# Performance work log

Measured on AMD Instinct MI355X. Metric: run time of the kernel, lower is better.

The kernel has to match this reference:

```python
import jax, jax.numpy as jnp
import numpy as np

N_NODES = 40000
N_EDGES = 640000
D = 128
BN_EPS = 1e-5


def setup_inputs() -> dict:
    key = jax.random.key(0)
    ks = jax.random.split(key, 8)
    h = jax.random.normal(ks[0], (N_NODES, D), dtype=jnp.float32)
    snorm_n = jax.random.uniform(ks[1], (N_NODES, 1), dtype=jnp.float32)
    W_self = jax.random.normal(ks[2], (D, D), dtype=jnp.float32) * 0.05
    W_neigh = jax.random.normal(ks[3], (D, D), dtype=jnp.float32) * 0.05
    b = jax.random.normal(ks[4], (D,), dtype=jnp.float32) * 0.05
    gamma = jnp.ones((D,), dtype=jnp.float32)
    beta = jnp.zeros((D,), dtype=jnp.float32)
    src = jax.random.randint(ks[5], (N_EDGES,), 0, N_NODES, dtype=jnp.int32)
    dst = jax.random.randint(ks[6], (N_EDGES,), 0, N_NODES, dtype=jnp.int32)
    return {"h": h, "snorm_n": snorm_n, "W_self": W_self, "W_neigh": W_neigh,
            "b": b, "gamma": gamma, "beta": beta, "src": src, "dst": dst}


def reference(h, snorm_n, W_self, W_neigh, b, gamma, beta, src, dst):
    h_in = h
    # --- SAGEConv (mean aggregator): mean over in-neighbors (src -> dst) ---
    msg = h[src]                                   # [E, D] irregular gather
    agg = jax.ops.segment_sum(msg, dst, num_segments=N_NODES)  # [N, D]
    deg = jax.ops.segment_sum(jnp.ones((N_EDGES,), h.dtype), dst,
                              num_segments=N_NODES)            # [N]
    h_neigh = agg / jnp.maximum(deg, 1.0)[:, None]
    out = h @ W_self + h_neigh @ W_neigh + b       # fc_self + fc_neigh + bias
    out = jax.nn.relu(out)                         # activation
    # --- graph norm ---
    out = out * snorm_n
    # --- batch norm (training-style batch statistics over nodes) ---
    mean = jnp.mean(out, axis=0)
    var = jnp.var(out, axis=0)
    out = (out - mean) * jax.lax.rsqrt(var + BN_EPS) * gamma + beta
    # --- residual ---
    return h_in + out
```

## Files before the change

### kernel.cpp

```cpp
#include <hip/hip_runtime.h>
#include <hip/hip_bf16.h>

constexpr int N_NODES = 40000;
constexpr int N_EDGES = 640000;
constexpr int D = 128;
constexpr float BN_EPS = 1e-5f;
constexpr int CAP = 128;
constexpr int NTILES = 1250;
constexpr int NCOLOR = 8;
constexpr int NODES_PER_COLOR = N_NODES / NCOLOR;
constexpr int FILL_BLOCKS = 2560;
constexpr int COLOR_STRIDE = (FILL_BLOCKS / NCOLOR) * 256;
constexpr int NREP = 8;

typedef __attribute__((ext_vector_type(8))) short short8;
typedef __attribute__((ext_vector_type(4))) float f32x4;
typedef __attribute__((ext_vector_type(2))) float f32x2;

__device__ __forceinline__ unsigned bf16_rne(float f) {
    unsigned b = __float_as_uint(f);
    return (b + 0x7FFFu + ((b >> 16) & 1u)) >> 16;
}
__device__ __forceinline__ float bflo(unsigned w) { return __uint_as_float(w << 16); }
__device__ __forceinline__ float bfhi(unsigned w) { return __uint_as_float(w & 0xFFFF0000u); }

__global__ __launch_bounds__(256) void cvt_fill_kernel(
        const int* __restrict__ dst,
        const int* __restrict__ src,
        int* __restrict__ cursor,
        int* __restrict__ esrc,
        const float4* __restrict__ h4,
        uint4* __restrict__ hb4,
        uint2* __restrict__ hb8,
        const float* __restrict__ Wself,
        const float* __restrict__ Wneigh,
        uint4* __restrict__ wfrag) {
    int gid = blockIdx.x * blockDim.x + threadIdx.x;

    if (gid < N_EDGES) {
        float4 a = h4[2 * gid];
        float4 b = h4[2 * gid + 1];
        uint4 o;
        o.x = bf16_rne(a.x) | (bf16_rne(a.y) << 16);
        o.y = bf16_rne(a.z) | (bf16_rne(a.w) << 16);
        o.z = bf16_rne(b.x) | (bf16_rne(b.y) << 16);
        o.w = bf16_rne(b.z) | (bf16_rne(b.w) << 16);
        hb4[gid] = o;
        unsigned w0 = __builtin_amdgcn_cvt_pk_fp8_f32(a.x, a.y, 0, false);
        w0 = __builtin_amdgcn_cvt_pk_fp8_f32(a.z, a.w, w0, true);
        unsigned w1 = __builtin_amdgcn_cvt_pk_fp8_f32(b.x, b.y, 0, false);
        w1 = __builtin_amdgcn_cvt_pk_fp8_f32(b.z, b.w, w1, true);
        uint2 o8; o8.x = w0; o8.y = w1;
        hb8[gid] = o8;
    }
    if (gid < 4096) {
        int G = gid;
        int l = G & 63;
        int tile = G >> 6;
        int kg = l >> 4, n = l & 15;
        int ct = tile >> 3, kt = tile & 7;
        int k0 = kt * 32 + kg * 8;
        int col = ct * 16 + n;
        unsigned w[8];
        #pragma unroll
        for (int j = 0; j < 8; j++) {
            int k = k0 + j;
            float v = (k < D) ? Wself[(size_t)k * D + col]
                              : Wneigh[(size_t)(k - D) * D + col];
            w[j] = bf16_rne(v);
        }
        uint4 ow;
        ow.x = w[0] | (w[1] << 16);
        ow.y = w[2] | (w[3] << 16);
        ow.z = w[4] | (w[5] << 16);
        ow.w = w[6] | (w[7] << 16);
        wfrag[G] = ow;
    }

    int c = blockIdx.x & (NCOLOR - 1);
    int lo = c * NODES_PER_COLOR;
    int hi = lo + NODES_PER_COLOR;
    int base = (blockIdx.x >> 3) * 256 + threadIdx.x;
    for (int e = base; e < N_EDGES; e += COLOR_STRIDE) {
        int t = dst[e];
        if (t >= lo && t < hi) {
            int s = src[e];
            int p = atomicAdd(&cursor[t], 1);
            if (p < CAP) esrc[t * CAP + p] = s;
        }
    }
}

__global__ __launch_bounds__(256) void gather_kernel(
        const uint4* __restrict__ hb8q,
        const int* __restrict__ cursor,
        const int* __restrict__ esrc,
        uint4* __restrict__ hnb4) {
    int c = blockIdx.x & (NCOLOR - 1);
    int rank = blockIdx.x >> 3;
    int wid = threadIdx.x >> 6;
    int node = c * NODES_PER_COLOR + rank * 4 + wid;
    int lane = threadIdx.x & 63;
    int g  = lane & 7;
    int es = lane >> 3;
    int deg = cursor[node];
    int cnt = deg < CAP ? deg : CAP;
    const int* bucket = esrc + node * CAP;
    float acc[16];
    #pragma unroll
    for (int i = 0; i < 16; i++) acc[i] = 0.f;
    for (int j = es; j < cnt; j += 8) {
        int a = bucket[j];
        uint4 v = hb8q[(size_t)a * 8 + g];
        f32x2 f;
        f = __builtin_amdgcn_cvt_pk_f32_fp8(v.x, false); acc[0]  += f.x; acc[1]  += f.y;
        f = __builtin_amdgcn_cvt_pk_f32_fp8(v.x, true);  acc[2]  += f.x; acc[3]  += f.y;
        f = __builtin_amdgcn_cvt_pk_f32_fp8(v.y, false); acc[4]  += f.x; acc[5]  += f.y;
        f = __builtin_amdgcn_cvt_pk_f32_fp8(v.y, true);  acc[6]  += f.x; acc[7]  += f.y;
        f = __builtin_amdgcn_cvt_pk_f32_fp8(v.z, false); acc[8]  += f.x; acc[9]  += f.y;
        f = __builtin_amdgcn_cvt_pk_f32_fp8(v.z, true);  acc[10] += f.x; acc[11] += f.y;
        f = __builtin_amdgcn_cvt_pk_f32_fp8(v.w, false); acc[12] += f.x; acc[13] += f.y;
        f = __builtin_amdgcn_cvt_pk_f32_fp8(v.w, true);  acc[14] += f.x; acc[15] += f.y;
    }
    #pragma unroll
    for (int i = 0; i < 16; i++) {
        acc[i] += __shfl_xor(acc[i], 8);
        acc[i] += __shfl_xor(acc[i], 16);
        acc[i] += __shfl_xor(acc[i], 32);
    }
    if (es == 0) {
        float rd = 1.0f / (float)(deg > 1 ? deg : 1);
        uint4 o0, o1;
        o0.x = bf16_rne(acc[0] * rd)  | (bf16_rne(acc[1] * rd)  << 16);
        o0.y = bf16_rne(acc[2] * rd)  | (bf16_rne(acc[3] * rd)  << 16);
        o0.z = bf16_rne(acc[4] * rd)  | (bf16_rne(acc[5] * rd)  << 16);
        o0.w = bf16_rne(acc[6] * rd)  | (bf16_rne(acc[7] * rd)  << 16);
        o1.x = bf16_rne(acc[8] * rd)  | (bf16_rne(acc[9] * rd)  << 16);
        o1.y = bf16_rne(acc[10] * rd) | (bf16_rne(acc[11] * rd) << 16);
        o1.z = bf16_rne(acc[12] * rd) | (bf16_rne(acc[13] * rd) << 16);
        o1.w = bf16_rne(acc[14] * rd) | (bf16_rne(acc[15] * rd) << 16);
        hnb4[(size_t)node * 16 + g * 2]     = o0;
        hnb4[(size_t)node * 16 + g * 2 + 1] = o1;
    }
}

__global__ __launch_bounds__(256) void gemm_kernel(
        const uint4* __restrict__ hb4,
        const uint4* __restrict__ hnb4,
        const uint4* __restrict__ wfrag,
        const float* __restrict__ snorm,
        const float* __restrict__ bias,
        ushort* __restrict__ preb,
        float* __restrict__ sums_r,
        float* __restrict__ sumsq_r) {
    __shared__ uint4 ldsW[2048];
    __shared__ float sums_l[64];
    __shared__ float sumsq_l[64];

    int t = threadIdx.x;
    int lane = t & 63;
    int wid = t >> 6;
    int n = lane & 15;
    int kg = lane >> 4;
    int rowtile = blockIdx.x >> 1;
    int cbt = blockIdx.x & 1;
    int cb = cbt * 64;
    int row_base = rowtile * 64 + wid * 16;
    int row = row_base + n;

    if (t < 64) { sums_l[t] = 0.f; sumsq_l[t] = 0.f; }

    short8 a[8];
    #pragma unroll
    for (int kt = 0; kt < 4; kt++) {
        uint4 v = hb4[(size_t)row * 16 + kt * 4 + kg];
        a[kt] = __builtin_bit_cast(short8, v);
    }
    #pragma unroll
    for (int kt = 0; kt < 4; kt++) {
        uint4 v = hnb4[(size_t)row * 16 + kt * 4 + kg];
        a[4 + kt] = __builtin_bit_cast(short8, v);
    }

    #pragma unroll
    for (int i = 0; i < 8; i++) {
        int g = i * 256 + t;
        ldsW[g] = wfrag[cbt * 2048 + g];
    }
    __syncthreads();

    f32x4 acc[4];
    #pragma unroll
    for (int lt = 0; lt < 4; lt++) acc[lt] = (f32x4){0.f, 0.f, 0.f, 0.f};
    #pragma unroll
    for (int lt = 0; lt < 4; lt++) {
        #pragma unroll
        for (int kt = 0; kt < 8; kt++) {
            short8 b = __builtin_bit_cast(short8, ldsW[(lt * 8 + kt) * 64 + lane]);
            acc[lt] = __builtin_amdgcn_mfma_f32_16x16x32_bf16(a[kt], b, acc[lt], 0, 0, 0);
        }
    }

    float snv[4];
    #pragma unroll
    for (int r = 0; r < 4; r++) snv[r] = snorm[row_base + kg * 4 + r];

    #pragma unroll
    for (int lt = 0; lt < 4; lt++) {
        int col = cb + lt * 16 + n;
        float bb = bias[col];
        float csum = 0.f, csq = 0.f;
        #pragma unroll
        for (int r = 0; r < 4; r++) {
            int rr = row_base + kg * 4 + r;
            float v = acc[lt][r] + bb;
            v = fmaxf(v, 0.f);
            v *= snv[r];
            preb[(size_t)rr * D + col] = (ushort)bf16_rne(v);
            csum += v;
            csq += v * v;
        }
        csum += __shfl_xor(csum, 16); csq += __shfl_xor(csq, 16);
        csum += __shfl_xor(csum, 32); csq += __shfl_xor(csq, 32);
        if (kg == 0) {
            atomicAdd(&sums_l[lt * 16 + n], csum);
            atomicAdd(&sumsq_l[lt * 16 + n], csq);
        }
    }
    __syncthreads();
    if (t < 64) {
        int rep = blockIdx.x & (NREP - 1);
        atomicAdd(&sums_r[rep * D + cb + t], sums_l[t]);
        atomicAdd(&sumsq_r[rep * D + cb + t], sumsq_l[t]);
    }
}

__global__ __launch_bounds__(256) void final_kernel(
        const float4* __restrict__ h4,
        const float4* __restrict__ sums_r4,
        const float4* __restrict__ sumsq_r4,
        const float4* __restrict__ gamma4,
        const float4* __restrict__ beta4,
        const uint4* __restrict__ preb4,
        float4* __restrict__ out4) {
    int idx = blockIdx.x * blockDim.x + threadIdx.x;
    int total = N_NODES * D / 8;
    if (idx >= total) return;
    int g = idx & 15;
    const float invN = 1.0f / (float)N_NODES;

    float4 s0 = {0.f,0.f,0.f,0.f}, s1 = {0.f,0.f,0.f,0.f};
    float4 q0 = {0.f,0.f,0.f,0.f}, q1 = {0.f,0.f,0.f,0.f};
    #pragma unroll
    for (int r = 0; r < NREP; r++) {
        float4 a0 = sums_r4[r * 32 + 2 * g],  a1 = sums_r4[r * 32 + 2 * g + 1];
        float4 c0 = sumsq_r4[r * 32 + 2 * g], c1 = sumsq_r4[r * 32 + 2 * g + 1];
        s0.x += a0.x; s0.y += a0.y; s0.z += a0.z; s0.w += a0.w;
        s1.x += a1.x; s1.y += a1.y; s1.z += a1.z; s1.w += a1.w;
        q0.x += c0.x; q0.y += c0.y; q0.z += c0.z; q0.w += c0.w;
        q1.x += c1.x; q1.y += c1.y; q1.z += c1.z; q1.w += c1.w;
    }

    float4 g0 = gamma4[2 * g], g1 = gamma4[2 * g + 1];
    float4 b0 = beta4[2 * g],  b1 = beta4[2 * g + 1];

    uint4 p = preb4[idx];
    float4 h0 = h4[2 * idx], h1 = h4[2 * idx + 1];
    float4 o0, o1;
    float m, var, sc;

    m = s0.x * invN; var = q0.x * invN - m * m; sc = g0.x * rsqrtf(var + BN_EPS);
    o0.x = h0.x + (bflo(p.x) - m) * sc + b0.x;
    m = s0.y * invN; var = q0.y * invN - m * m; sc = g0.y * rsqrtf(var + BN_EPS);
    o0.y = h0.y + (bfhi(p.x) - m) * sc + b0.y;
    m = s0.z * invN; var = q0.z * invN - m * m; sc = g0.z * rsqrtf(var + BN_EPS);
    o0.z = h0.z + (bflo(p.y) - m) * sc + b0.z;
    m = s0.w * invN; var = q0.w * invN - m * m; sc = g0.w * rsqrtf(var + BN_EPS);
    o0.w = h0.w + (bfhi(p.y) - m) * sc + b0.w;

    m = s1.x * invN; var = q1.x * invN - m * m; sc = g1.x * rsqrtf(var + BN_EPS);
    o1.x = h1.x + (bflo(p.z) - m) * sc + b1.x;
    m = s1.y * invN; var = q1.y * invN - m * m; sc = g1.y * rsqrtf(var + BN_EPS);
    o1.y = h1.y + (bfhi(p.z) - m) * sc + b1.y;
    m = s1.z * invN; var = q1.z * invN - m * m; sc = g1.z * rsqrtf(var + BN_EPS);
    o1.z = h1.z + (bflo(p.w) - m) * sc + b1.z;
    m = s1.w * invN; var = q1.w * invN - m * m; sc = g1.w * rsqrtf(var + BN_EPS);
    o1.w = h1.w + (bfhi(p.w) - m) * sc + b1.w;

    out4[2 * idx]     = o0;
    out4[2 * idx + 1] = o1;
}

extern "C" void kernel_launch(void* const* d_in, const int* in_sizes, int n_in,
                              void* d_out, int out_size, void* d_ws, size_t ws_size,
                              hipStream_t stream) {
    const float* h      = (const float*)d_in[0];
    const float* snorm  = (const float*)d_in[1];
    const float* Wself  = (const float*)d_in[2];
    const float* Wneigh = (const float*)d_in[3];
    const float* bias   = (const float*)d_in[4];
    const float* gamma  = (const float*)d_in[5];
    const float* beta   = (const float*)d_in[6];
    const int*   src    = (const int*)d_in[7];
    const int*   dst    = (const int*)d_in[8];
    float* out = (float*)d_out;

    int*   cursor  = (int*)d_ws;
    float* sums_r  = (float*)(cursor + N_NODES);
    float* sumsq_r = sums_r + NREP * D;
    int*   esrc    = (int*)(sumsq_r + NREP * D);
    size_t off     = (size_t)((char*)(esrc + (size_t)N_NODES * CAP) - (char*)d_ws);
    off = (off + 15) & ~(size_t)15;
    uint4* wfrag = (uint4*)((char*)d_ws + off);
    uint4* hb4   = wfrag + 4096;
    uint4* hnb4  = hb4 + N_NODES * (D / 8);
    ushort* preb = (ushort*)(hnb4 + N_NODES * (D / 8));
    uint2* hb8   = (uint2*)(preb + (size_t)N_NODES * D);

    size_t zero_bytes = (size_t)(N_NODES + 2 * NREP * D) * sizeof(float);
    hipMemsetAsync(d_ws, 0, zero_bytes, stream);

    cvt_fill_kernel<<<FILL_BLOCKS, 256, 0, stream>>>(
        dst, src, cursor, esrc, (const float4*)h, hb4, hb8, Wself, Wneigh, wfrag);
    gather_kernel<<<N_NODES / 4, 256, 0, stream>>>(
        (const uint4*)hb8, cursor, esrc, hnb4);
    gemm_kernel<<<NTILES, 256, 0, stream>>>(hb4, hnb4, wfrag, snorm, bias,
                                            preb, sums_r, sumsq_r);
    final_kernel<<<(N_NODES * D / 8 + 255) / 256, 256, 0, stream>>>(
        (const float4*)h, (const float4*)sums_r, (const float4*)sumsq_r,
        (const float4*)gamma, (const float4*)beta, (const uint4*)preb,
        (float4*)out);
}
```

Before: 169.0 us.

## Fuse neighbor gather into GEMM kernel via LDS tile, dropping hnb intermediate

Merges the gather and GEMM kernels into one. Each block of 16 nodes aggregates its neighbor means into a shared-memory tile, then runs the bf16 MFMA GEMM over all 128 output columns. This removes the global write and re-read of the aggregated neighbor matrix and one kernel launch. In exchange the GEMM now reads W fragments straight from global memory instead of staging them in LDS, and the gather loses the color-based block ordering. The number of BN-stat replicas is doubled to spread the atomic contention.

```diff
diff --git a/kernel.cpp b/kernel.cpp
--- a/kernel.cpp
+++ b/kernel.cpp
@@ -6,12 +6,12 @@
 constexpr int D = 128;
 constexpr float BN_EPS = 1e-5f;
 constexpr int CAP = 128;
-constexpr int NTILES = 1250;
 constexpr int NCOLOR = 8;
 constexpr int NODES_PER_COLOR = N_NODES / NCOLOR;
 constexpr int FILL_BLOCKS = 2560;
 constexpr int COLOR_STRIDE = (FILL_BLOCKS / NCOLOR) * 256;
-constexpr int NREP = 8;
+constexpr int NREP = 16;
+constexpr int GG_BLOCKS = N_NODES / 16;
 
 typedef __attribute__((ext_vector_type(8))) short short8;
 typedef __attribute__((ext_vector_type(4))) float f32x4;
@@ -91,113 +91,100 @@
     }
 }
 
-__global__ __launch_bounds__(256) void gather_kernel(
+__global__ __launch_bounds__(256) void gather_gemm_kernel(
+        const uint4* __restrict__ hb4,
         const uint4* __restrict__ hb8q,
         const int* __restrict__ cursor,
         const int* __restrict__ esrc,
-        uint4* __restrict__ hnb4) {
-    int c = blockIdx.x & (NCOLOR - 1);
-    int rank = blockIdx.x >> 3;
-    int wid = threadIdx.x >> 6;
-    int node = c * NODES_PER_COLOR + rank * 4 + wid;
-    int lane = threadIdx.x & 63;
-    int g  = lane & 7;
-    int es = lane >> 3;
-    int deg = cursor[node];
-    int cnt = deg < CAP ? deg : CAP;
-    const int* bucket = esrc + node * CAP;
-    float acc[16];
-    #pragma unroll
-    for (int i = 0; i < 16; i++) acc[i] = 0.f;
-    for (int j = es; j < cnt; j += 8) {
-        int a = bucket[j];
-        uint4 v = hb8q[(size_t)a * 8 + g];
-        f32x2 f;
-        f = __builtin_amdgcn_cvt_pk_f32_fp8(v.x, false); acc[0]  += f.x; acc[1]  += f.y;
-        f = __builtin_amdgcn_cvt_pk_f32_fp8(v.x, true);  acc[2]  += f.x; acc[3]  += f.y;
-        f = __builtin_amdgcn_cvt_pk_f32_fp8(v.y, false); acc[4]  += f.x; acc[5]  += f.y;
-        f = __builtin_amdgcn_cvt_pk_f32_fp8(v.y, true);  acc[6]  += f.x; acc[7]  += f.y;
-        f = __builtin_amdgcn_cvt_pk_f32_fp8(v.z, false); acc[8]  += f.x; acc[9]  += f.y;
-        f = __builtin_amdgcn_cvt_pk_f32_fp8(v.z, true);  acc[10] += f.x; acc[11] += f.y;
-        f = __builtin_amdgcn_cvt_pk_f32_fp8(v.w, false); acc[12] += f.x; acc[13] += f.y;
-        f = __builtin_amdgcn_cvt_pk_f32_fp8(v.w, true);  acc[14] += f.x; acc[15] += f.y;
-    }
-    #pragma unroll
-    for (int i = 0; i < 16; i++) {
-        acc[i] += __shfl_xor(acc[i], 8);
-        acc[i] += __shfl_xor(acc[i], 16);
-        acc[i] += __shfl_xor(acc[i], 32);
-    }
-    if (es == 0) {
-        float rd = 1.0f / (float)(deg > 1 ? deg : 1);
-        uint4 o0, o1;
-        o0.x = bf16_rne(acc[0] * rd)  | (bf16_rne(acc[1] * rd)  << 16);
-        o0.y = bf16_rne(acc[2] * rd)  | (bf16_rne(acc[3] * rd)  << 16);
-        o0.z = bf16_rne(acc[4] * rd)  | (bf16_rne(acc[5] * rd)  << 16);
-        o0.w = bf16_rne(acc[6] * rd)  | (bf16_rne(acc[7] * rd)  << 16);
-        o1.x = bf16_rne(acc[8] * rd)  | (bf16_rne(acc[9] * rd)  << 16);
-        o1.y = bf16_rne(acc[10] * rd) | (bf16_rne(acc[11] * rd) << 16);
-        o1.z = bf16_rne(acc[12] * rd) | (bf16_rne(acc[13] * rd) << 16);
-        o1.w = bf16_rne(acc[14] * rd) | (bf16_rne(acc[15] * rd) << 16);
-        hnb4[(size_t)node * 16 + g * 2]     = o0;
-        hnb4[(size_t)node * 16 + g * 2 + 1] = o1;
-    }
-}
-
-__global__ __launch_bounds__(256) void gemm_kernel(
-        const uint4* __restrict__ hb4,
-        const uint4* __restrict__ hnb4,
         const uint4* __restrict__ wfrag,
         const float* __restrict__ snorm,
         const float* __restrict__ bias,
         ushort* __restrict__ preb,
         float* __restrict__ sums_r,
         float* __restrict__ sumsq_r) {
-    __shared__ uint4 ldsW[2048];
-    __shared__ float sums_l[64];
-    __shared__ float sumsq_l[64];
+    __shared__ uint4 ntile[16][17];
+    __shared__ float sums_l[128];
+    __shared__ float sumsq_l[128];
 
     int t = threadIdx.x;
     int lane = t & 63;
-    int wid = t >> 6;
-    int n = lane & 15;
+    int w = t >> 6;
+    int row_base = blockIdx.x * 16;
+
+    if (t < 128) { sums_l[t] = 0.f; sumsq_l[t] = 0.f; }
+
+    int n  = lane & 15;
     int kg = lane >> 4;
-    int rowtile = blockIdx.x >> 1;
-    int cbt = blockIdx.x & 1;
-    int cb = cbt * 64;
-    int row_base = rowtile * 64 + wid * 16;
     int row = row_base + n;
-
-    if (t < 64) { sums_l[t] = 0.f; sumsq_l[t] = 0.f; }
-
-    short8 a[8];
-    #pragma unroll
-    for (int kt = 0; kt < 4; kt++) {
-        uint4 v = hb4[(size_t)row * 16 + kt * 4 + kg];
-        a[kt] = __builtin_bit_cast(short8, v);
-    }
-    #pragma unroll
-    for (int kt = 0; kt < 4; kt++) {
-        uint4 v = hnb4[(size_t)row * 16 + kt * 4 + kg];
-        a[4 + kt] = __builtin_bit_cast(short8, v);
-    }
-
-    #pragma unroll
-    for (int i = 0; i < 8; i++) {
-        int g = i * 256 + t;
-        ldsW[g] = wfrag[cbt * 2048 + g];
+    uint4 a_s[4];
+    #pragma unroll
+    for (int kt = 0; kt < 4; kt++)
+        a_s[kt] = hb4[(size_t)row * 16 + kt * 4 + kg];
+
+    int g  = lane & 7;
+    int es = lane >> 3;
+    #pragma unroll
+    for (int i = 0; i < 4; i++) {
+        int node = row_base + w * 4 + i;
+        int deg = cursor[node];
+        int cnt = deg < CAP ? deg : CAP;
+        const int* bucket = esrc + node * CAP;
+        float acc[16];
+        #pragma unroll
+        for (int q = 0; q < 16; q++) acc[q] = 0.f;
+        for (int j = es; j < cnt; j += 8) {
+            int a = bucket[j];
+            uint4 v = hb8q[(size_t)a * 8 + g];
+            f32x2 f;
+            f = __builtin_amdgcn_cvt_pk_f32_fp8(v.x, false); acc[0]  += f.x; acc[1]  += f.y;
+            f = __builtin_amdgcn_cvt_pk_f32_fp8(v.x, true);  acc[2]  += f.x; acc[3]  += f.y;
+            f = __builtin_amdgcn_cvt_pk_f32_fp8(v.y, false); acc[4]  += f.x; acc[5]  += f.y;
+            f = __builtin_amdgcn_cvt_pk_f32_fp8(v.y, true);  acc[6]  += f.x; acc[7]  += f.y;
+            f = __builtin_amdgcn_cvt_pk_f32_fp8(v.z, false); acc[8]  += f.x; acc[9]  += f.y;
+            f = __builtin_amdgcn_cvt_pk_f32_fp8(v.z, true);  acc[10] += f.x; acc[11] += f.y;
+            f = __builtin_amdgcn_cvt_pk_f32_fp8(v.w, false); acc[12] += f.x; acc[13] += f.y;
+            f = __builtin_amdgcn_cvt_pk_f32_fp8(v.w, true);  acc[14] += f.x; acc[15] += f.y;
+        }
+        #pragma unroll
+        for (int q = 0; q < 16; q++) {
+            acc[q] += __shfl_xor(acc[q], 8);
+            acc[q] += __shfl_xor(acc[q], 16);
+            acc[q] += __shfl_xor(acc[q], 32);
+        }
+        if (es == 0) {
+            float rd = 1.0f / (float)(deg > 1 ? deg : 1);
+            uint4 o0, o1;
+            o0.x = bf16_rne(acc[0] * rd)  | (bf16_rne(acc[1] * rd)  << 16);
+            o0.y = bf16_rne(acc[2] * rd)  | (bf16_rne(acc[3] * rd)  << 16);
+            o0.z = bf16_rne(acc[4] * rd)  | (bf16_rne(acc[5] * rd)  << 16);
+            o0.w = bf16_rne(acc[6] * rd)  | (bf16_rne(acc[7] * rd)  << 16);
+            o1.x = bf16_rne(acc[8] * rd)  | (bf16_rne(acc[9] * rd)  << 16);
+            o1.y = bf16_rne(acc[10] * rd) | (bf16_rne(acc[11] * rd) << 16);
+            o1.z = bf16_rne(acc[12] * rd) | (bf16_rne(acc[13] * rd) << 16);
+            o1.w = bf16_rne(acc[14] * rd) | (bf16_rne(acc[15] * rd) << 16);
+            int rloc = w * 4 + i;
+            ntile[rloc][g * 2]     = o0;
+            ntile[rloc][g * 2 + 1] = o1;
+        }
     }
     __syncthreads();
 
-    f32x4 acc[4];
-    #pragma unroll
-    for (int lt = 0; lt < 4; lt++) acc[lt] = (f32x4){0.f, 0.f, 0.f, 0.f};
-    #pragma unroll
-    for (int lt = 0; lt < 4; lt++) {
+    uint4 a_n[4];
+    #pragma unroll
+    for (int kt = 0; kt < 4; kt++)
+        a_n[kt] = ntile[n][kt * 4 + kg];
+
+    f32x4 acc2[2];
+    acc2[0] = (f32x4){0.f, 0.f, 0.f, 0.f};
+    acc2[1] = (f32x4){0.f, 0.f, 0.f, 0.f};
+    #pragma unroll
+    for (int ct = 0; ct < 2; ct++) {
+        int CT = w * 2 + ct;
         #pragma unroll
         for (int kt = 0; kt < 8; kt++) {
-            short8 b = __builtin_bit_cast(short8, ldsW[(lt * 8 + kt) * 64 + lane]);
-            acc[lt] = __builtin_amdgcn_mfma_f32_16x16x32_bf16(a[kt], b, acc[lt], 0, 0, 0);
+            short8 b = __builtin_bit_cast(short8, wfrag[(CT * 8 + kt) * 64 + lane]);
+            short8 a = __builtin_bit_cast(short8, (kt < 4) ? a_s[kt] : a_n[kt - 4]);
+            acc2[ct] = __builtin_amdgcn_mfma_f32_16x16x32_bf16(a, b, acc2[ct], 0, 0, 0);
         }
     }
 
@@ -206,14 +193,14 @@
     for (int r = 0; r < 4; r++) snv[r] = snorm[row_base + kg * 4 + r];
 
     #pragma unroll
-    for (int lt = 0; lt < 4; lt++) {
-        int col = cb + lt * 16 + n;
+    for (int ct = 0; ct < 2; ct++) {
+        int col = w * 32 + ct * 16 + n;
         float bb = bias[col];
         float csum = 0.f, csq = 0.f;
         #pragma unroll
         for (int r = 0; r < 4; r++) {
             int rr = row_base + kg * 4 + r;
-            float v = acc[lt][r] + bb;
+            float v = acc2[ct][r] + bb;
             v = fmaxf(v, 0.f);
             v *= snv[r];
             preb[(size_t)rr * D + col] = (ushort)bf16_rne(v);
@@ -223,15 +210,15 @@
         csum += __shfl_xor(csum, 16); csq += __shfl_xor(csq, 16);
         csum += __shfl_xor(csum, 32); csq += __shfl_xor(csq, 32);
         if (kg == 0) {
-            atomicAdd(&sums_l[lt * 16 + n], csum);
-            atomicAdd(&sumsq_l[lt * 16 + n], csq);
+            atomicAdd(&sums_l[col], csum);
+            atomicAdd(&sumsq_l[col], csq);
         }
     }
     __syncthreads();
-    if (t < 64) {
+    if (t < 128) {
         int rep = blockIdx.x & (NREP - 1);
-        atomicAdd(&sums_r[rep * D + cb + t], sums_l[t]);
-        atomicAdd(&sumsq_r[rep * D + cb + t], sumsq_l[t]);
+        atomicAdd(&sums_r[rep * D + t], sums_l[t]);
+        atomicAdd(&sumsq_r[rep * D + t], sumsq_l[t]);
     }
 }
 
@@ -313,8 +300,7 @@
     off = (off + 15) & ~(size_t)15;
     uint4* wfrag = (uint4*)((char*)d_ws + off);
     uint4* hb4   = wfrag + 4096;
-    uint4* hnb4  = hb4 + N_NODES * (D / 8);
-    ushort* preb = (ushort*)(hnb4 + N_NODES * (D / 8));
+    ushort* preb = (ushort*)(hb4 + N_NODES * (D / 8));
     uint2* hb8   = (uint2*)(preb + (size_t)N_NODES * D);
 
     size_t zero_bytes = (size_t)(N_NODES + 2 * NREP * D) * sizeof(float);
@@ -322,10 +308,9 @@
 
     cvt_fill_kernel<<<FILL_BLOCKS, 256, 0, stream>>>(
         dst, src, cursor, esrc, (const float4*)h, hb4, hb8, Wself, Wneigh, wfrag);
-    gather_kernel<<<N_NODES / 4, 256, 0, stream>>>(
-        (const uint4*)hb8, cursor, esrc, hnb4);
-    gemm_kernel<<<NTILES, 256, 0, stream>>>(hb4, hnb4, wfrag, snorm, bias,
-                                            preb, sums_r, sumsq_r);
+    gather_gemm_kernel<<<GG_BLOCKS, 256, 0, stream>>>(
+        hb4, (const uint4*)hb8, cursor, esrc, wfrag, snorm, bias,
+        preb, sums_r, sumsq_r);
     final_kernel<<<(N_NODES * D / 8 + 255) / 256, 256, 0, stream>>>(
         (const float4*)h, (const float4*)sums_r, (const float4*)sumsq_r,
         (const float4*)gamma, (const float4*)beta, (const uint4*)preb,
```

Result: slower. 180.3 us (+6.7%).

## Fuse GEMM and batch-norm finalize into one persistent kernel with grid barrier

Applied to the files above, without the earlier changes.

Merges the GEMM and final normalization kernels into one kernel of 625 blocks. Each block computes two tiles, keeps the activations in registers, and waits at a global atomic-counter barrier until all column statistics are accumulated. It then applies the batch-norm scale and shift plus the residual directly. This removes the bf16 intermediate write and re-read and one kernel launch. In exchange it relies on all 625 blocks being co-resident (launch bounds of 3 blocks per CU), adds spin-wait latency, and uses uncoalesced scalar fp32 stores for the output. NREP for the atomic replicas rises from 8 to 16.

```diff
diff --git a/kernel.cpp b/kernel.cpp
--- a/kernel.cpp
+++ b/kernel.cpp
@@ -11,7 +11,8 @@
 constexpr int NODES_PER_COLOR = N_NODES / NCOLOR;
 constexpr int FILL_BLOCKS = 2560;
 constexpr int COLOR_STRIDE = (FILL_BLOCKS / NCOLOR) * 256;
-constexpr int NREP = 8;
+constexpr int NREP = 16;
+constexpr int FGRID = 625;
 
 typedef __attribute__((ext_vector_type(8))) short short8;
 typedef __attribute__((ext_vector_type(4))) float f32x4;
@@ -144,151 +145,169 @@
     }
 }
 
-__global__ __launch_bounds__(256) void gemm_kernel(
+__device__ __forceinline__ void compute_tile(
+        int tile, int t, int lane, int wid, int n, int kg, int rep,
         const uint4* __restrict__ hb4,
         const uint4* __restrict__ hnb4,
         const uint4* __restrict__ wfrag,
         const float* __restrict__ snorm,
         const float* __restrict__ bias,
-        ushort* __restrict__ preb,
         float* __restrict__ sums_r,
-        float* __restrict__ sumsq_r) {
+        float* __restrict__ sumsq_r,
+        uint4* ldsW, float* sums_l, float* sumsq_l,
+        float (&v)[16]) {
+    int rowtile = tile >> 1;
+    int cbt = tile & 1;
+    int cb = cbt * 64;
+    int row_base = rowtile * 64 + wid * 16;
+    int row = row_base + n;
+
+    if (t < 64) { sums_l[t] = 0.f; sumsq_l[t] = 0.f; }
+    #pragma unroll
+    for (int i = 0; i < 8; i++) {
+        int g = i * 256 + t;
+        ldsW[g] = wfrag[cbt * 2048 + g];
+    }
+
+    short8 a[8];
+    #pragma unroll
+    for (int kt = 0; kt < 4; kt++)
+        a[kt] = __builtin_bit_cast(short8, hb4[(size_t)row * 16 + kt * 4 + kg]);
+    #pragma unroll
+    for (int kt = 0; kt < 4; kt++)
+        a[4 + kt] = __builtin_bit_cast(short8, hnb4[(size_t)row * 16 + kt * 4 + kg]);
+
+    __syncthreads();
+
+    f32x4 acc[4];
+    #pragma unroll
+    for (int lt = 0; lt < 4; lt++) acc[lt] = (f32x4){0.f, 0.f, 0.f, 0.f};
+    #pragma unroll
+    for (int lt = 0; lt < 4; lt++) {
+        #pragma unroll
+        for (int kt = 0; kt < 8; kt++) {
+            short8 b = __builtin_bit_cast(short8, ldsW[(lt * 8 + kt) * 64 + lane]);
+            acc[lt] = __builtin_amdgcn_mfma_f32_16x16x32_bf16(a[kt], b, acc[lt], 0, 0, 0);
+        }
+    }
+
+    float snv[4];
+    #pragma unroll
+    for (int r = 0; r < 4; r++) snv[r] = snorm[row_base + kg * 4 + r];
+
+    #pragma unroll
+    for (int lt = 0; lt < 4; lt++) {
+        int col = cb + lt * 16 + n;
+        float bb = bias[col];
+        float csum = 0.f, csq = 0.f;
+        #pragma unroll
+        for (int r = 0; r < 4; r++) {
+            float x = acc[lt][r] + bb;
+            x = fmaxf(x, 0.f);
+            x *= snv[r];
+            v[lt * 4 + r] = x;
+            csum += x;
+            csq += x * x;
+        }
+        csum += __shfl_xor(csum, 16); csq += __shfl_xor(csq, 16);
+        csum += __shfl_xor(csum, 32); csq += __shfl_xor(csq, 32);
+        if (kg == 0) {
+            atomicAdd(&sums_l[lt * 16 + n], csum);
+            atomicAdd(&sumsq_l[lt * 16 + n], csq);
+        }
+    }
+    __syncthreads();
+    if (t < 64) {
+        atomicAdd(&sums_r[rep * D + cb + t], sums_l[t]);
+        atomicAdd(&sumsq_r[rep * D + cb + t], sumsq_l[t]);
+    }
+    __syncthreads();
+}
+
+__global__ __launch_bounds__(256, 3) void gemm_final_kernel(
+        const uint4* __restrict__ hb4,
+        const uint4* __restrict__ hnb4,
+        const uint4* __restrict__ wfrag,
+        const float* __restrict__ snorm,
+        const float* __restrict__ bias,
+        const float* __restrict__ gamma,
+        const float* __restrict__ beta,
+        const float* __restrict__ h,
+        float* __restrict__ sums_r,
+        float* __restrict__ sumsq_r,
+        int* __restrict__ done,
+        float* __restrict__ out) {
     __shared__ uint4 ldsW[2048];
     __shared__ float sums_l[64];
     __shared__ float sumsq_l[64];
+    __shared__ float colA[128];
+    __shared__ float colB[128];
 
     int t = threadIdx.x;
     int lane = t & 63;
     int wid = t >> 6;
     int n = lane & 15;
     int kg = lane >> 4;
-    int rowtile = blockIdx.x >> 1;
-    int cbt = blockIdx.x & 1;
-    int cb = cbt * 64;
-    int row_base = rowtile * 64 + wid * 16;
-    int row = row_base + n;
-
-    if (t < 64) { sums_l[t] = 0.f; sumsq_l[t] = 0.f; }
-
-    short8 a[8];
-    #pragma unroll
-    for (int kt = 0; kt < 4; kt++) {
-        uint4 v = hb4[(size_t)row * 16 + kt * 4 + kg];
-        a[kt] = __builtin_bit_cast(short8, v);
-    }
-    #pragma unroll
-    for (int kt = 0; kt < 4; kt++) {
-        uint4 v = hnb4[(size_t)row * 16 + kt * 4 + kg];
-        a[4 + kt] = __builtin_bit_cast(short8, v);
-    }
-
-    #pragma unroll
-    for (int i = 0; i < 8; i++) {
-        int g = i * 256 + t;
-        ldsW[g] = wfrag[cbt * 2048 + g];
-    }
-    __syncthreads();
-
-    f32x4 acc[4];
-    #pragma unroll
-    for (int lt = 0; lt < 4; lt++) acc[lt] = (f32x4){0.f, 0.f, 0.f, 0.f};
-    #pragma unroll
-    for (int lt = 0; lt < 4; lt++) {
-        #pragma unroll
-        for (int kt = 0; kt < 8; kt++) {
-            short8 b = __builtin_bit_cast(short8, ldsW[(lt * 8 + kt) * 64 + lane]);
-            acc[lt] = __builtin_amdgcn_mfma_f32_16x16x32_bf16(a[kt], b, acc[lt], 0, 0, 0);
-        }
-    }
-
-    float snv[4];
-    #pragma unroll
-    for (int r = 0; r < 4; r++) snv[r] = snorm[row_base + kg * 4 + r];
-
-    #pragma unroll
-    for (int lt = 0; lt < 4; lt++) {
-        int col = cb + lt * 16 + n;
-        float bb = bias[col];
-        float csum = 0.f, csq = 0.f;
-        #pragma unroll
-        for (int r = 0; r < 4; r++) {
-            int rr = row_base + kg * 4 + r;
-            float v = acc[lt][r] + bb;
-            v = fmaxf(v, 0.f);
-            v *= snv[r];
-            preb[(size_t)rr * D + col] = (ushort)bf16_rne(v);
-            csum += v;
-            csq += v * v;
-        }
-        csum += __shfl_xor(csum, 16); csq += __shfl_xor(csq, 16);
-        csum += __shfl_xor(csum, 32); csq += __shfl_xor(csq, 32);
-        if (kg == 0) {
-            atomicAdd(&sums_l[lt * 16 + n], csum);
-            atomicAdd(&sumsq_l[lt * 16 + n], csq);
-        }
-    }
-    __syncthreads();
-    if (t < 64) {
-        int rep = blockIdx.x & (NREP - 1);
-        atomicAdd(&sums_r[rep * D + cb + t], sums_l[t]);
-        atomicAdd(&sumsq_r[rep * D + cb + t], sumsq_l[t]);
-    }
-}
-
-__global__ __launch_bounds__(256) void final_kernel(
-        const float4* __restrict__ h4,
-        const float4* __restrict__ sums_r4,
-        const float4* __restrict__ sumsq_r4,
-        const float4* __restrict__ gamma4,
-        const float4* __restrict__ beta4,
-        const uint4* __restrict__ preb4,
-        float4* __restrict__ out4) {
-    int idx = blockIdx.x * blockDim.x + threadIdx.x;
-    int total = N_NODES * D / 8;
-    if (idx >= total) return;
-    int g = idx & 15;
-    const float invN = 1.0f / (float)N_NODES;
-
-    float4 s0 = {0.f,0.f,0.f,0.f}, s1 = {0.f,0.f,0.f,0.f};
-    float4 q0 = {0.f,0.f,0.f,0.f}, q1 = {0.f,0.f,0.f,0.f};
-    #pragma unroll
-    for (int r = 0; r < NREP; r++) {
-        float4 a0 = sums_r4[r * 32 + 2 * g],  a1 = sums_r4[r * 32 + 2 * g + 1];
-        float4 c0 = sumsq_r4[r * 32 + 2 * g], c1 = sumsq_r4[r * 32 + 2 * g + 1];
-        s0.x += a0.x; s0.y += a0.y; s0.z += a0.z; s0.w += a0.w;
-        s1.x += a1.x; s1.y += a1.y; s1.z += a1.z; s1.w += a1.w;
-        q0.x += c0.x; q0.y += c0.y; q0.z += c0.z; q0.w += c0.w;
-        q1.x += c1.x; q1.y += c1.y; q1.z += c1.z; q1.w += c1.w;
-    }
-
-    float4 g0 = gamma4[2 * g], g1 = gamma4[2 * g + 1];
-    float4 b0 = beta4[2 * g],  b1 = beta4[2 * g + 1];
-
-    uint4 p = preb4[idx];
-    float4 h0 = h4[2 * idx], h1 = h4[2 * idx + 1];
-    float4 o0, o1;
-    float m, var, sc;
-
-    m = s0.x * invN; var = q0.x * invN - m * m; sc = g0.x * rsqrtf(var + BN_EPS);
-    o0.x = h0.x + (bflo(p.x) - m) * sc + b0.x;
-    m = s0.y * invN; var = q0.y * invN - m * m; sc = g0.y * rsqrtf(var + BN_EPS);
-    o0.y = h0.y + (bfhi(p.x) - m) * sc + b0.y;
-    m = s0.z * invN; var = q0.z * invN - m * m; sc = g0.z * rsqrtf(var + BN_EPS);
-    o0.z = h0.z + (bflo(p.y) - m) * sc + b0.z;
-    m = s0.w * invN; var = q0.w * invN - m * m; sc = g0.w * rsqrtf(var + BN_EPS);
-    o0.w = h0.w + (bfhi(p.y) - m) * sc + b0.w;
-
-    m = s1.x * invN; var = q1.x * invN - m * m; sc = g1.x * rsqrtf(var + BN_EPS);
-    o1.x = h1.x + (bflo(p.z) - m) * sc + b1.x;
-    m = s1.y * invN; var = q1.y * invN - m * m; sc = g1.y * rsqrtf(var + BN_EPS);
-    o1.y = h1.y + (bfhi(p.z) - m) * sc + b1.y;
-    m = s1.z * invN; var = q1.z * invN - m * m; sc = g1.z * rsqrtf(var + BN_EPS);
-    o1.z = h1.z + (bflo(p.w) - m) * sc + b1.z;
-    m = s1.w * invN; var = q1.w * invN - m * m; sc = g1.w * rsqrtf(var + BN_EPS);
-    o1.w = h1.w + (bfhi(p.w) - m) * sc + b1.w;
-
-    out4[2 * idx]     = o0;
-    out4[2 * idx + 1] = o1;
+    int rep = blockIdx.x & (NREP - 1);
+
+    int tile0 = blockIdx.x;
+    int tile1 = blockIdx.x + FGRID;
+
+    float v0[16], v1[16];
+    compute_tile(tile0, t, lane, wid, n, kg, rep, hb4, hnb4, wfrag, snorm,
+                 bias, sums_r, sumsq_r, ldsW, sums_l, sumsq_l, v0);
+    compute_tile(tile1, t, lane, wid, n, kg, rep, hb4, hnb4, wfrag, snorm,
+                 bias, sums_r, sumsq_r, ldsW, sums_l, sumsq_l, v1);
+
+    __threadfence();
+    __syncthreads();
+    if (t == 0) {
+        __hip_atomic_fetch_add(done, 1, __ATOMIC_ACQ_REL,
+                               __HIP_MEMORY_SCOPE_AGENT);
+        while (__hip_atomic_load(done, __ATOMIC_ACQUIRE,
+                                 __HIP_MEMORY_SCOPE_AGENT) < FGRID)
+            __builtin_amdgcn_s_sleep(8);
+    }
+    __syncthreads();
+
+    if (t < 128) {
+        float s = 0.f, q = 0.f;
+        #pragma unroll
+        for (int r = 0; r < NREP; r++) {
+            s += __hip_atomic_load(&sums_r[r * D + t], __ATOMIC_RELAXED,
+                                   __HIP_MEMORY_SCOPE_AGENT);
+            q += __hip_atomic_load(&sumsq_r[r * D + t], __ATOMIC_RELAXED,
+                                   __HIP_MEMORY_SCOPE_AGENT);
+        }
+        const float invN = 1.0f / (float)N_NODES;
+        float m = s * invN;
+        float var = q * invN - m * m;
+        float sc = gamma[t] * rsqrtf(var + BN_EPS);
+        colA[t] = sc;
+        colB[t] = beta[t] - m * sc;
+    }
+    __syncthreads();
+
+    #pragma unroll
+    for (int half = 0; half < 2; half++) {
+        int tile = half == 0 ? tile0 : tile1;
+        const float (&v)[16] = half == 0 ? v0 : v1;
+        int rowtile = tile >> 1;
+        int cb = (tile & 1) * 64;
+        int row_base = rowtile * 64 + wid * 16;
+        #pragma unroll
+        for (int lt = 0; lt < 4; lt++) {
+            int col = cb + lt * 16 + n;
+            float A = colA[col];
+            float B = colB[col];
+            #pragma unroll
+            for (int r = 0; r < 4; r++) {
+                int rr = row_base + kg * 4 + r;
+                out[(size_t)rr * D + col] =
+                    h[(size_t)rr * D + col] + v[lt * 4 + r] * A + B;
+            }
+        }
+    }
 }
 
 extern "C" void kernel_launch(void* const* d_in, const int* in_sizes, int n_in,
@@ -308,26 +327,23 @@
     int*   cursor  = (int*)d_ws;
     float* sums_r  = (float*)(cursor + N_NODES);
     float* sumsq_r = sums_r + NREP * D;
-    int*   esrc    = (int*)(sumsq_r + NREP * D);
+    int*   done    = (int*)(sumsq_r + NREP * D);
+    int*   esrc    = done + 1;
     size_t off     = (size_t)((char*)(esrc + (size_t)N_NODES * CAP) - (char*)d_ws);
     off = (off + 15) & ~(size_t)15;
     uint4* wfrag = (uint4*)((char*)d_ws + off);
     uint4* hb4   = wfrag + 4096;
     uint4* hnb4  = hb4 + N_NODES * (D / 8);
-    ushort* preb = (ushort*)(hnb4 + N_NODES * (D / 8));
-    uint2* hb8   = (uint2*)(preb + (size_t)N_NODES * D);
-
-    size_t zero_bytes = (size_t)(N_NODES + 2 * NREP * D) * sizeof(float);
+    uint2* hb8   = (uint2*)(hnb4 + N_NODES * (D / 8));
+
+    size_t zero_bytes = (size_t)(N_NODES + 2 * NREP * D + 1) * sizeof(float);
     hipMemsetAsync(d_ws, 0, zero_bytes, stream);
 
     cvt_fill_kernel<<<FILL_BLOCKS, 256, 0, stream>>>(
         dst, src, cursor, esrc, (const float4*)h, hb4, hb8, Wself, Wneigh, wfrag);
     gather_kernel<<<N_NODES / 4, 256, 0, stream>>>(
         (const uint4*)hb8, cursor, esrc, hnb4);
-    gemm_kernel<<<NTILES, 256, 0, stream>>>(hb4, hnb4, wfrag, snorm, bias,
-                                            preb, sums_r, sumsq_r);
-    final_kernel<<<(N_NODES * D / 8 + 255) / 256, 256, 0, stream>>>(
-        (const float4*)h, (const float4*)sums_r, (const float4*)sumsq_r,
-        (const float4*)gamma, (const float4*)beta, (const uint4*)preb,
-        (float4*)out);
-}
+    gemm_final_kernel<<<FGRID, 256, 0, stream>>>(
+        hb4, hnb4, wfrag, snorm, bias, gamma, beta, h,
+        sums_r, sumsq_r, done, out);
+}
```

Result: slower. 279.2 us (+65.2%).
